# Optimization experiments

Hardware: AMD Instinct MI355X
Metric: run time of the kernel (lower is better)

## Reference

```python
import jax, jax.numpy as jnp
import numpy as np

B, N, NC = 16, 25200, 80          # batch, raw predictions, classes (COCO)
CONF_THRES = 0.25
IOU_THRES = 0.45
MAX_CAND = 1000                    # candidates kept after score top-k (pre-NMS)
CLS_OFFSET = 4096.0                # class-wise box offset (non-agnostic NMS trick)
EPS = 1e-7


def setup_inputs() -> dict:
    key = jax.random.key(0)
    # raw head output: [x, y, w, h, obj, cls0..cls79], values in [0,1]
    pred = jax.random.uniform(key, (B, N, 5 + NC), dtype=jnp.float32)
    return {"pred": pred}


def _xywh2xyxy(x):
    xy, wh = x[..., :2], x[..., 2:4]
    return jnp.concatenate([xy - wh * 0.5, xy + wh * 0.5], axis=-1)


def _box_iou(boxes):
    # boxes: [C, 4] xyxy -> pairwise IoU [C, C]
    area = (boxes[:, 2] - boxes[:, 0]) * (boxes[:, 3] - boxes[:, 1])
    lt = jnp.maximum(boxes[:, None, :2], boxes[None, :, :2])
    rb = jnp.minimum(boxes[:, None, 2:], boxes[None, :, 2:])
    wh = jnp.clip(rb - lt, 0.0)
    inter = wh[..., 0] * wh[..., 1]
    return inter / (area[:, None] + area[None, :] - inter + EPS)


def _nms_single(p):
    # p: [N, 5+NC] -> (out [MAX_CAND, 6] xyxy/conf/cls zero-padded, keep [MAX_CAND] bool)
    obj = p[:, 4]
    cls_scores = p[:, 5:] * obj[:, None]          # conf = obj * cls
    conf = jnp.max(cls_scores, axis=-1)
    cls_idx = jnp.argmax(cls_scores, axis=-1)
    valid = (obj > CONF_THRES) & (conf > CONF_THRES)
    score = jnp.where(valid, conf, -1.0)

    # pre-NMS top-k by score (sorted descending) — fixed-shape stand-in for boolean filter
    top_scores, idx = jax.lax.top_k(score, MAX_CAND)
    boxes = _xywh2xyxy(p[idx, :4])                # [C, 4]
    kconf = conf[idx]
    kcls = cls_idx[idx].astype(jnp.float32)
    valid_c = top_scores > 0.0

    # class-offset boxes so different classes never overlap (agnostic=False)
    off_boxes = boxes + kcls[:, None] * CLS_OFFSET
    iou = _box_iou(off_boxes)                     # [C, C]

    ar = jnp.arange(MAX_CAND)

    def body(i, keep):
        sup = keep[i] & (iou[i] > IOU_THRES) & (ar > i)
        return keep & jnp.logical_not(sup)

    keep = jax.lax.fori_loop(0, MAX_CAND, body, valid_c)

    out = jnp.concatenate([boxes, kconf[:, None], kcls[:, None]], axis=-1)  # [C, 6]
    out = jnp.where(keep[:, None], out, 0.0)
    return out, keep


def reference(pred):
    out, keep = jax.vmap(_nms_single)(pred)
    return out, keep
```

## Files before the change

kernel.cpp:

```cpp
#include <hip/hip_runtime.h>
#include <stdint.h>

typedef unsigned int u32;
typedef unsigned long long u64;

#define BATCH 16
#define NANCH 25200
#define NCLS 80
#define ROWF 85
#define MAXC 1000
#define CONF_T 0.25f
#define IOU_T 0.45f
#define EPS_F 1e-7f
#define TILE 64
#define NTILES ((NANCH + TILE - 1) / TILE)

__device__ __forceinline__ float iou_ref(float4 a, float4 b) {
#pragma clang fp contract(off)
  float ai = (a.z - a.x) * (a.w - a.y);
  float aj = (b.z - b.x) * (b.w - b.y);
  float ltx = fmaxf(a.x, b.x), lty = fmaxf(a.y, b.y);
  float rbx = fminf(a.z, b.z), rby = fminf(a.w, b.w);
  float wx = fmaxf(rbx - ltx, 0.0f), wy = fmaxf(rby - lty, 0.0f);
  float inter = wx * wy;
  return inter / (ai + aj - inter + EPS_F);
}

__global__ __launch_bounds__(256) void k1_score(const float* __restrict__ pred,
                                                u32* __restrict__ keys32) {
  __shared__ float srow[TILE * ROWF];
  __shared__ u32 skeys[TILE];
  int tid = threadIdx.x;
  int b = blockIdx.y;
  int t0 = blockIdx.x * TILE;
  int ntile = (t0 + TILE <= NANCH) ? TILE : (NANCH - t0);
  int nf4 = (ntile * ROWF) >> 2;

  const float4* src4 = (const float4*)(pred + ((size_t)b * NANCH + t0) * ROWF);
  float4* smem4 = (float4*)srow;
#pragma unroll
  for (int k = 0; k < 6; ++k) {
    int i = k * 256 + tid;
    if (i < nf4) smem4[i] = src4[i];
  }
  __syncthreads();

  int a = tid >> 2;
  int q = tid & 3;
  float best = -1e30f;
  int bidx = 0;
  float obj = 0.0f;
  if (a < ntile) {
    const float* row = srow + a * ROWF;
    obj = row[4];
    int c0 = q * 20;
#pragma unroll
    for (int c = 0; c < 20; ++c) {
      float s = row[5 + c0 + c] * obj;
      if (s > best) { best = s; bidx = c0 + c; }
    }
  }
#pragma unroll
  for (int off = 1; off < 4; off <<= 1) {
    float ob = __shfl_xor(best, off);
    int oi = __shfl_xor(bidx, off);
    if (ob > best || (ob == best && oi < bidx)) { best = ob; bidx = oi; }
  }
  if (q == 0 && a < ntile) {
    bool valid = (obj > CONF_T) && (best > CONF_T);
    u32 k = valid ? (((__float_as_uint(best) - 0x3E800000u) << 7) | (u32)bidx)
                  : 0u;
    skeys[a] = k;
  }
  __syncthreads();
  if (tid < ntile) keys32[(size_t)b * NANCH + t0 + tid] = skeys[tid];
}

__global__ __launch_bounds__(1024) void k2_select(const float* __restrict__ pred,
                                                  const u32* __restrict__ keys32,
                                                  float* __restrict__ selbox,
                                                  float* __restrict__ offbox,
                                                  float2* __restrict__ selmeta) {
  int b = blockIdx.x;
  int tid = threadIdx.x;
  int wv = tid >> 6, lane = tid & 63;
  __shared__ u32 h[8192];
  __shared__ u64 skey[2048];
  __shared__ u32 wsum[16];
  __shared__ u32 sh_fbin;
  __shared__ u32 scount;

  const u32* kb = keys32 + (size_t)b * NANCH;
  u32 kreg[25];
#pragma unroll
  for (int j = 0; j < 25; ++j) {
    int i = tid + j * 1024;
    kreg[j] = (i < NANCH) ? kb[i] : 0u;
  }
  for (int i = tid; i < 8192; i += 1024) h[i] = 0;
  if (tid == 0) { sh_fbin = 0; scount = 0; }
  skey[tid] = ~0ull;
  skey[tid + 1024] = ~0ull;
  __syncthreads();
#pragma unroll
  for (int j = 0; j < 25; ++j) {
    u32 k = kreg[j];
    if (k >= 0x80u) atomicAdd(&h[k >> 18], 1u);
  }
  __syncthreads();
  u32 a[8]; u32 lsum = 0;
#pragma unroll
  for (int k = 0; k < 8; ++k) { a[k] = h[8 * tid + k]; lsum += a[k]; }
  u32 suf = lsum;
#pragma unroll
  for (int off = 1; off < 64; off <<= 1) {
    u32 tv = __shfl_down(suf, off);
    if (lane + off < 64) suf += tv;
  }
  if (lane == 0) wsum[wv] = suf;
  __syncthreads();
  u32 base = 0;
#pragma unroll
  for (int w2 = 0; w2 < 16; ++w2) if (w2 > wv) base += wsum[w2];
  u32 e = base + suf - lsum;
#pragma unroll
  for (int k = 7; k >= 0; --k) {
    u32 inc = e + a[k];
    if ((int)inc >= MAXC && (int)e < MAXC) sh_fbin = (u32)(8 * tid + k);
    e = inc;
  }
  __syncthreads();
  u32 cut = sh_fbin << 18;
#pragma unroll
  for (int j = 0; j < 25; ++j) {
    u32 k = kreg[j];
    bool take = (k >= cut) && (k != 0u);
    u64 mask = __ballot(take ? 1 : 0);
    u32 wbase = 0;
    if (lane == 0 && mask != 0ull)
      wbase = atomicAdd(&scount, (u32)__popcll(mask));
    wbase = (u32)__shfl((int)wbase, 0);
    if (take) {
      int i = tid + j * 1024;
      u64 sk = ((u64)(k >> 7) << 32) |
               (u64)(((32767u - (u32)i) << 7) | (k & 127u));
      u32 p = wbase + (u32)__popcll(mask & ((1ull << lane) - 1ull));
      if (p < 2048) skey[p] = ~sk;
    }
  }
  __syncthreads();
  u64 v;
  if (scount <= 1024u) {
    v = skey[tid];
    for (u32 kk = 2; kk <= 1024; kk <<= 1) {
      for (u32 j = kk >> 1; j > 0; j >>= 1) {
        bool up = ((tid & kk) == 0);
        bool low = ((tid & j) == 0);
        if (j >= 64) {
          skey[tid] = v;
          __syncthreads();
          u64 o = skey[tid ^ j];
          bool takemin = (up == low);
          v = takemin ? (v < o ? v : o) : (v > o ? v : o);
          __syncthreads();
        } else {
          u64 o = __shfl_xor(v, (int)j);
          bool takemin = (up == low);
          v = takemin ? (v < o ? v : o) : (v > o ? v : o);
        }
      }
    }
  } else {
    for (u32 kk = 2; kk <= 2048; kk <<= 1) {
      for (u32 j = kk >> 1; j > 0; j >>= 1) {
        for (int idx = tid; idx < 2048; idx += 1024) {
          u32 ixj = (u32)idx ^ j;
          if (ixj > (u32)idx) {
            u64 x = skey[idx], y = skey[ixj];
            bool up = ((idx & kk) == 0);
            if (up ? (x > y) : (x < y)) { skey[idx] = y; skey[ixj] = x; }
          }
        }
        __syncthreads();
      }
    }
    v = skey[tid];
  }
  if (tid < MAXC) {
    u64 k = ~v;
    u32 confpart = (u32)(k >> 32);
    u32 lo = (u32)k;
    bool valid = confpart != 0u;
    float conf = 0.0f, x1 = 0.0f, y1 = 0.0f, x2 = 0.0f, y2 = 0.0f;
    float cf = 0.0f, offv = 0.0f;
    if (valid) {
      u32 nidx = 32767u - ((lo >> 7) & 0x7FFFu);
      u32 ci = lo & 127u;
      conf = __uint_as_float(confpart + 0x3E800000u);
      const float* pr = pred + ((size_t)b * NANCH + nidx) * ROWF;
      float x = pr[0], y = pr[1], w = pr[2], h2 = pr[3];
      x1 = x - w * 0.5f; y1 = y - h2 * 0.5f;
      x2 = x + w * 0.5f; y2 = y + h2 * 0.5f;
      cf = (float)ci; offv = cf * 4096.0f;
    }
    int o = b * MAXC + tid;
    ((float4*)selbox)[o] = make_float4(x1, y1, x2, y2);
    ((float4*)offbox)[o] = make_float4(x1 + offv, y1 + offv, x2 + offv, y2 + offv);
    selmeta[o] = make_float2(conf, cf);
  }
}

__global__ __launch_bounds__(256) void k3_dt(const float4* __restrict__ offbox4,
                                             u64* __restrict__ dt) {
  int wid = blockIdx.x * 4 + (threadIdx.x >> 6);
  int lane = threadIdx.x & 63;
  int b = wid / MAXC;
  int i = wid % MAXC;
  float4 bi = offbox4[b * MAXC + i];
  u64 myword = 0;
  int wmax = i >> 6;
  for (int w = 0; w <= wmax; ++w) {
    int j = w * 64 + lane;
    int jc = (j < MAXC) ? j : 0;
    float4 bj = offbox4[b * MAXC + jc];
    float iou = iou_ref(bi, bj);
    bool bit = (iou > IOU_T) && (j < i);
    u64 bal = __ballot(bit ? 1 : 0);
    if (lane == w) myword = bal;
  }
  if (lane < 16) dt[((size_t)b * 16 + lane) * MAXC + i] = myword;
}

__global__ __launch_bounds__(1024) void k4_jacobi(const u64* __restrict__ dt,
                                                  const float2* __restrict__ selmeta,
                                                  const float* __restrict__ selbox,
                                                  float* __restrict__ out) {
  int b = blockIdx.x;
  int tid = threadIdx.x;
  int wv = tid >> 6, lane = tid & 63;
  __shared__ u64 keepv[16];
  __shared__ u32 changed2[2];
  bool valid = false;
  float2 meta = make_float2(0.0f, 0.0f);
  u64 dtr[16];
  if (tid < MAXC) {
    meta = selmeta[b * MAXC + tid];
    valid = meta.x > 0.0f;
#pragma unroll
    for (int w = 0; w < 16; ++w) dtr[w] = dt[((size_t)b * 16 + w) * MAXC + tid];
  } else {
#pragma unroll
    for (int w = 0; w < 16; ++w) dtr[w] = 0ull;
  }
  u64 bal0 = __ballot(valid ? 1 : 0);
  if (tid == 0) { changed2[0] = 0; changed2[1] = 0; }
  if (lane == 0) keepv[wv] = bal0;
  __syncthreads();
  for (int pass = 0; pass < MAXC; ++pass) {
    u64 kv[16];
#pragma unroll
    for (int w = 0; w < 16; ++w) kv[w] = keepv[w];
    u64 s = 0;
#pragma unroll
    for (int w = 0; w < 16; ++w) s |= dtr[w] & kv[w];
    bool nk = valid && (s == 0ull);
    u64 bal = __ballot(nk ? 1 : 0);
    __syncthreads();
    if (lane == 0 && bal != kv[wv]) {
      keepv[wv] = bal;
      atomicOr(&changed2[pass & 1], 1u);
    }
    __syncthreads();
    u32 ch = changed2[pass & 1];
    if (tid == 0) changed2[(pass & 1) ^ 1] = 0;
    if (!ch) break;
  }
  if (tid < MAXC) {
    bool kept = ((keepv[wv] >> lane) & 1ull) != 0ull;
    size_t o = (size_t)b * MAXC + tid;
    float4 bx = ((const float4*)selbox)[o];
    float* orow = out + o * 6;
    orow[0] = kept ? bx.x : 0.0f;
    orow[1] = kept ? bx.y : 0.0f;
    orow[2] = kept ? bx.z : 0.0f;
    orow[3] = kept ? bx.w : 0.0f;
    orow[4] = kept ? meta.x : 0.0f;
    orow[5] = kept ? meta.y : 0.0f;
    out[(size_t)BATCH * MAXC * 6 + o] = kept ? 1.0f : 0.0f;
  }
}

extern "C" void kernel_launch(void* const* d_in, const int* in_sizes, int n_in,
                              void* d_out, int out_size, void* d_ws, size_t ws_size,
                              hipStream_t stream) {
  const float* pred = (const float*)d_in[0];
  float* out = (float*)d_out;
  char* ws = (char*)d_ws;
  size_t off = 0;
  auto alloc = [&](size_t bytes) -> void* {
    void* p = ws + off;
    off = (off + bytes + 255) & ~(size_t)255;
    return p;
  };
  u32* keys32   = (u32*)alloc((size_t)BATCH * NANCH * 4);
  float* selbox = (float*)alloc((size_t)BATCH * MAXC * 4 * 4);
  float* offbox = (float*)alloc((size_t)BATCH * MAXC * 4 * 4);
  float2* selmeta = (float2*)alloc((size_t)BATCH * MAXC * 8);
  u64* dt       = (u64*)alloc((size_t)BATCH * 16 * MAXC * 8);
  (void)ws_size; (void)in_sizes; (void)n_in; (void)out_size;

  dim3 g1(NTILES, BATCH);
  k1_score<<<g1, 256, 0, stream>>>(pred, keys32);
  k2_select<<<BATCH, 1024, 0, stream>>>(pred, keys32, selbox, offbox, selmeta);
  k3_dt<<<(BATCH * MAXC) / 4, 256, 0, stream>>>((const float4*)offbox, dt);
  k4_jacobi<<<BATCH, 1024, 0, stream>>>(dt, selmeta, selbox, out);
}
```

Measured before the change: 238.2 us.

## Fuse four NMS kernels into one cooperative persistent kernel with grid syncs

Replaces the four separate launches (score, select/sort, IoU bitmask, Jacobi keep iteration) with a single cooperative kernel of 256 blocks of 1024 threads, separated by grid.sync barriers. The aim is to remove per-launch overhead and inter-kernel gaps. In exchange, the score stage now runs with fewer, larger blocks, and the select and Jacobi stages still use only 16 blocks while the rest of the grid waits at the barrier. If the cooperative launch fails, it falls back to the old four-kernel path.

```diff
diff --git a/kernel.cpp b/kernel.cpp
--- a/kernel.cpp
+++ b/kernel.cpp
@@ -1,5 +1,8 @@
 #include <hip/hip_runtime.h>
+#include <hip/hip_cooperative_groups.h>
 #include <stdint.h>
+
+namespace cg = cooperative_groups;
 
 typedef unsigned int u32;
 typedef unsigned long long u64;
@@ -12,6 +15,13 @@
 #define CONF_T 0.25f
 #define IOU_T 0.45f
 #define EPS_F 1e-7f
+
+#define MBLK 1024
+#define MGRID 256
+#define TILE_A 256
+#define TPB ((NANCH + TILE_A - 1) / TILE_A)
+#define TT (TPB * BATCH)
+
 #define TILE 64
 #define NTILES ((NANCH + TILE - 1) / TILE)
 
@@ -26,6 +36,269 @@
   return inter / (ai + aj - inter + EPS_F);
 }
 
+struct SMa { float srow[TILE_A * ROWF]; u32 skeys[TILE_A]; };
+struct SMb { u32 h[8192]; u64 skey[2048]; u32 wsum[16]; u32 sh_fbin; u32 scount; };
+struct SMd { u64 keepv[16]; u32 changed2[2]; };
+union SMU { SMa a; SMb b; SMd d; };
+
+__global__ __launch_bounds__(MBLK) void mega(const float* __restrict__ pred,
+                                             u32* __restrict__ keys32,
+                                             float* __restrict__ selbox,
+                                             float* __restrict__ offbox,
+                                             float2* __restrict__ selmeta,
+                                             u64* __restrict__ dt,
+                                             float* __restrict__ out) {
+  cg::grid_group grid = cg::this_grid();
+  __shared__ SMU sm;
+  int tid = threadIdx.x;
+  int wv = tid >> 6, lane = tid & 63;
+
+  {
+    float4* smem4 = (float4*)sm.a.srow;
+    for (int t = blockIdx.x; t < TT; t += MGRID) {
+      int b = t / TPB;
+      int ti = t - b * TPB;
+      int t0 = ti * TILE_A;
+      int ntile = (t0 + TILE_A <= NANCH) ? TILE_A : (NANCH - t0);
+      int nf4 = (ntile * ROWF) >> 2;
+      const float4* src4 = (const float4*)(pred + ((size_t)b * NANCH + t0) * ROWF);
+      for (int i = tid; i < nf4; i += MBLK) smem4[i] = src4[i];
+      __syncthreads();
+      int a = tid >> 2;
+      int q = tid & 3;
+      float best = -1e30f;
+      int bidx = 0;
+      float obj = 0.0f;
+      if (a < ntile) {
+        const float* row = sm.a.srow + a * ROWF;
+        obj = row[4];
+        int c0 = q * 20;
+#pragma unroll
+        for (int c = 0; c < 20; ++c) {
+          float s = row[5 + c0 + c] * obj;
+          if (s > best) { best = s; bidx = c0 + c; }
+        }
+      }
+#pragma unroll
+      for (int off = 1; off < 4; off <<= 1) {
+        float ob = __shfl_xor(best, off);
+        int oi = __shfl_xor(bidx, off);
+        if (ob > best || (ob == best && oi < bidx)) { best = ob; bidx = oi; }
+      }
+      if (q == 0 && a < ntile) {
+        bool valid = (obj > CONF_T) && (best > CONF_T);
+        sm.a.skeys[a] = valid
+            ? (((__float_as_uint(best) - 0x3E800000u) << 7) | (u32)bidx) : 0u;
+      }
+      __syncthreads();
+      if (tid < ntile) keys32[(size_t)b * NANCH + t0 + tid] = sm.a.skeys[tid];
+      __syncthreads();
+    }
+  }
+  __threadfence();
+  grid.sync();
+
+  if (blockIdx.x < BATCH) {
+    int b = blockIdx.x;
+    const u32* kb = keys32 + (size_t)b * NANCH;
+    u32 kreg[25];
+#pragma unroll
+    for (int j = 0; j < 25; ++j) {
+      int i = tid + j * 1024;
+      kreg[j] = (i < NANCH) ? kb[i] : 0u;
+    }
+    for (int i = tid; i < 8192; i += 1024) sm.b.h[i] = 0;
+    if (tid == 0) { sm.b.sh_fbin = 0; sm.b.scount = 0; }
+    sm.b.skey[tid] = ~0ull;
+    sm.b.skey[tid + 1024] = ~0ull;
+    __syncthreads();
+#pragma unroll
+    for (int j = 0; j < 25; ++j) {
+      u32 k = kreg[j];
+      if (k >= 0x80u) atomicAdd(&sm.b.h[k >> 18], 1u);
+    }
+    __syncthreads();
+    u32 a[8]; u32 lsum = 0;
+#pragma unroll
+    for (int k = 0; k < 8; ++k) { a[k] = sm.b.h[8 * tid + k]; lsum += a[k]; }
+    u32 suf = lsum;
+#pragma unroll
+    for (int off = 1; off < 64; off <<= 1) {
+      u32 tv = __shfl_down(suf, off);
+      if (lane + off < 64) suf += tv;
+    }
+    if (lane == 0) sm.b.wsum[wv] = suf;
+    __syncthreads();
+    u32 base = 0;
+#pragma unroll
+    for (int w2 = 0; w2 < 16; ++w2) if (w2 > wv) base += sm.b.wsum[w2];
+    u32 e = base + suf - lsum;
+#pragma unroll
+    for (int k = 7; k >= 0; --k) {
+      u32 inc = e + a[k];
+      if ((int)inc >= MAXC && (int)e < MAXC) sm.b.sh_fbin = (u32)(8 * tid + k);
+      e = inc;
+    }
+    __syncthreads();
+    u32 cut = sm.b.sh_fbin << 18;
+#pragma unroll
+    for (int j = 0; j < 25; ++j) {
+      u32 k = kreg[j];
+      bool take = (k >= cut) && (k != 0u);
+      u64 mask = __ballot(take ? 1 : 0);
+      u32 wbase = 0;
+      if (lane == 0 && mask != 0ull)
+        wbase = atomicAdd(&sm.b.scount, (u32)__popcll(mask));
+      wbase = (u32)__shfl((int)wbase, 0);
+      if (take) {
+        int i = tid + j * 1024;
+        u64 sk = ((u64)(k >> 7) << 32) |
+                 (u64)(((32767u - (u32)i) << 7) | (k & 127u));
+        u32 p = wbase + (u32)__popcll(mask & ((1ull << lane) - 1ull));
+        if (p < 2048) sm.b.skey[p] = ~sk;
+      }
+    }
+    __syncthreads();
+    u64 v;
+    if (sm.b.scount <= 1024u) {
+      v = sm.b.skey[tid];
+      for (u32 kk = 2; kk <= 1024; kk <<= 1) {
+        for (u32 j = kk >> 1; j > 0; j >>= 1) {
+          bool up = ((tid & kk) == 0);
+          bool low = ((tid & j) == 0);
+          if (j >= 64) {
+            sm.b.skey[tid] = v;
+            __syncthreads();
+            u64 o = sm.b.skey[tid ^ j];
+            bool takemin = (up == low);
+            v = takemin ? (v < o ? v : o) : (v > o ? v : o);
+            __syncthreads();
+          } else {
+            u64 o = __shfl_xor(v, (int)j);
+            bool takemin = (up == low);
+            v = takemin ? (v < o ? v : o) : (v > o ? v : o);
+          }
+        }
+      }
+    } else {
+      for (u32 kk = 2; kk <= 2048; kk <<= 1) {
+        for (u32 j = kk >> 1; j > 0; j >>= 1) {
+          for (int idx = tid; idx < 2048; idx += 1024) {
+            u32 ixj = (u32)idx ^ j;
+            if (ixj > (u32)idx) {
+              u64 x = sm.b.skey[idx], y = sm.b.skey[ixj];
+              bool up = ((idx & kk) == 0);
+              if (up ? (x > y) : (x < y)) { sm.b.skey[idx] = y; sm.b.skey[ixj] = x; }
+            }
+          }
+          __syncthreads();
+        }
+      }
+      v = sm.b.skey[tid];
+    }
+    if (tid < MAXC) {
+      u64 k = ~v;
+      u32 confpart = (u32)(k >> 32);
+      u32 lo = (u32)k;
+      bool valid = confpart != 0u;
+      float conf = 0.0f, x1 = 0.0f, y1 = 0.0f, x2 = 0.0f, y2 = 0.0f;
+      float cf = 0.0f, offv = 0.0f;
+      if (valid) {
+        u32 nidx = 32767u - ((lo >> 7) & 0x7FFFu);
+        u32 ci = lo & 127u;
+        conf = __uint_as_float(confpart + 0x3E800000u);
+        const float* pr = pred + ((size_t)b * NANCH + nidx) * ROWF;
+        float x = pr[0], y = pr[1], w = pr[2], h2 = pr[3];
+        x1 = x - w * 0.5f; y1 = y - h2 * 0.5f;
+        x2 = x + w * 0.5f; y2 = y + h2 * 0.5f;
+        cf = (float)ci; offv = cf * 4096.0f;
+      }
+      int o = b * MAXC + tid;
+      ((float4*)selbox)[o] = make_float4(x1, y1, x2, y2);
+      ((float4*)offbox)[o] = make_float4(x1 + offv, y1 + offv, x2 + offv, y2 + offv);
+      selmeta[o] = make_float2(conf, cf);
+    }
+  }
+  __threadfence();
+  grid.sync();
+
+  {
+    const float4* offbox4 = (const float4*)offbox;
+    for (int wid = blockIdx.x * 16 + wv; wid < BATCH * MAXC; wid += MGRID * 16) {
+      int b = wid / MAXC;
+      int i = wid - b * MAXC;
+      float4 bi = offbox4[b * MAXC + i];
+      u64 myword = 0;
+      int wmax = i >> 6;
+      for (int w = 0; w <= wmax; ++w) {
+        int j = w * 64 + lane;
+        int jc = (j < MAXC) ? j : 0;
+        float4 bj = offbox4[b * MAXC + jc];
+        float iou = iou_ref(bi, bj);
+        bool bit = (iou > IOU_T) && (j < i);
+        u64 bal = __ballot(bit ? 1 : 0);
+        if (lane == w) myword = bal;
+      }
+      if (lane < 16) dt[((size_t)b * 16 + lane) * MAXC + i] = myword;
+    }
+  }
+  __threadfence();
+  grid.sync();
+
+  if (blockIdx.x < BATCH) {
+    int b = blockIdx.x;
+    bool valid = false;
+    float2 meta = make_float2(0.0f, 0.0f);
+    u64 dtr[16];
+    if (tid < MAXC) {
+      meta = selmeta[b * MAXC + tid];
+      valid = meta.x > 0.0f;
+#pragma unroll
+      for (int w = 0; w < 16; ++w) dtr[w] = dt[((size_t)b * 16 + w) * MAXC + tid];
+    } else {
+#pragma unroll
+      for (int w = 0; w < 16; ++w) dtr[w] = 0ull;
+    }
+    u64 bal0 = __ballot(valid ? 1 : 0);
+    if (tid == 0) { sm.d.changed2[0] = 0; sm.d.changed2[1] = 0; }
+    if (lane == 0) sm.d.keepv[wv] = bal0;
+    __syncthreads();
+    for (int pass = 0; pass < MAXC; ++pass) {
+      u64 kv[16];
+#pragma unroll
+      for (int w = 0; w < 16; ++w) kv[w] = sm.d.keepv[w];
+      u64 s = 0;
+#pragma unroll
+      for (int w = 0; w < 16; ++w) s |= dtr[w] & kv[w];
+      bool nk = valid && (s == 0ull);
+      u64 bal = __ballot(nk ? 1 : 0);
+      __syncthreads();
+      if (lane == 0 && bal != kv[wv]) {
+        sm.d.keepv[wv] = bal;
+        atomicOr(&sm.d.changed2[pass & 1], 1u);
+      }
+      __syncthreads();
+      u32 ch = sm.d.changed2[pass & 1];
+      if (tid == 0) sm.d.changed2[(pass & 1) ^ 1] = 0;
+      if (!ch) break;
+    }
+    if (tid < MAXC) {
+      bool kept = ((sm.d.keepv[wv] >> lane) & 1ull) != 0ull;
+      size_t o = (size_t)b * MAXC + tid;
+      float4 bx = ((const float4*)selbox)[o];
+      float* orow = out + o * 6;
+      orow[0] = kept ? bx.x : 0.0f;
+      orow[1] = kept ? bx.y : 0.0f;
+      orow[2] = kept ? bx.z : 0.0f;
+      orow[3] = kept ? bx.w : 0.0f;
+      orow[4] = kept ? meta.x : 0.0f;
+      orow[5] = kept ? meta.y : 0.0f;
+      out[(size_t)BATCH * MAXC * 6 + o] = kept ? 1.0f : 0.0f;
+    }
+  }
+}
+
+
 __global__ __launch_bounds__(256) void k1_score(const float* __restrict__ pred,
                                                 u32* __restrict__ keys32) {
   __shared__ float srow[TILE * ROWF];
@@ -35,7 +308,6 @@
   int t0 = blockIdx.x * TILE;
   int ntile = (t0 + TILE <= NANCH) ? TILE : (NANCH - t0);
   int nf4 = (ntile * ROWF) >> 2;
-
   const float4* src4 = (const float4*)(pred + ((size_t)b * NANCH + t0) * ROWF);
   float4* smem4 = (float4*)srow;
 #pragma unroll
@@ -44,9 +316,7 @@
     if (i < nf4) smem4[i] = src4[i];
   }
   __syncthreads();
-
-  int a = tid >> 2;
-  int q = tid & 3;
+  int a = tid >> 2, q = tid & 3;
   float best = -1e30f;
   int bidx = 0;
   float obj = 0.0f;
@@ -68,9 +338,7 @@
   }
   if (q == 0 && a < ntile) {
     bool valid = (obj > CONF_T) && (best > CONF_T);
-    u32 k = valid ? (((__float_as_uint(best) - 0x3E800000u) << 7) | (u32)bidx)
-                  : 0u;
-    skeys[a] = k;
+    skeys[a] = valid ? (((__float_as_uint(best) - 0x3E800000u) << 7) | (u32)bidx) : 0u;
   }
   __syncthreads();
   if (tid < ntile) keys32[(size_t)b * NANCH + t0 + tid] = skeys[tid];
@@ -89,7 +357,6 @@
   __shared__ u32 wsum[16];
   __shared__ u32 sh_fbin;
   __shared__ u32 scount;
-
   const u32* kb = keys32 + (size_t)b * NANCH;
   u32 kreg[25];
 #pragma unroll
@@ -309,9 +576,15 @@
   u64* dt       = (u64*)alloc((size_t)BATCH * 16 * MAXC * 8);
   (void)ws_size; (void)in_sizes; (void)n_in; (void)out_size;
 
-  dim3 g1(NTILES, BATCH);
-  k1_score<<<g1, 256, 0, stream>>>(pred, keys32);
-  k2_select<<<BATCH, 1024, 0, stream>>>(pred, keys32, selbox, offbox, selmeta);
-  k3_dt<<<(BATCH * MAXC) / 4, 256, 0, stream>>>((const float4*)offbox, dt);
-  k4_jacobi<<<BATCH, 1024, 0, stream>>>(dt, selmeta, selbox, out);
-}
+  void* args[] = { (void*)&pred, (void*)&keys32, (void*)&selbox, (void*)&offbox,
+                   (void*)&selmeta, (void*)&dt, (void*)&out };
+  hipError_t err = hipLaunchCooperativeKernel((const void*)mega, dim3(MGRID),
+                                              dim3(MBLK), args, 0, stream);
+  if (err != hipSuccess) {
+    dim3 g1(NTILES, BATCH);
+    k1_score<<<g1, 256, 0, stream>>>(pred, keys32);
+    k2_select<<<BATCH, 1024, 0, stream>>>(pred, keys32, selbox, offbox, selmeta);
+    k3_dt<<<(BATCH * MAXC) / 4, 256, 0, stream>>>((const float4*)offbox, dt);
+    k4_jacobi<<<BATCH, 1024, 0, stream>>>(dt, selmeta, selbox, out);
+  }
+}
```

New measurement: 564.8 us. 137% more time.

## Fuse select, IoU bitmask, and Jacobi NMS kernels into one per-batch kernel

Applied to the files above, without the earlier changes.

Merges the top-k selection, IoU suppression-matrix construction, and iterative keep-mask kernels into a single 1024-thread block per batch image. Boxes and the suppression bitmask now stay in shared memory (union-overlaid with the selection scratch), and box/meta values stay in registers instead of going through global workspace buffers. This removes two kernel launches and the global round trips, but the IoU matrix is now built by only 16 waves per batch on 16 blocks rather than spread across 4000 blocks. The large shared footprint (~147KB) also limits occupancy.

```diff
diff --git a/kernel.cpp b/kernel.cpp
--- a/kernel.cpp
+++ b/kernel.cpp
@@ -76,19 +76,19 @@
   if (tid < ntile) keys32[(size_t)b * NANCH + t0 + tid] = skeys[tid];
 }
 
-__global__ __launch_bounds__(1024) void k2_select(const float* __restrict__ pred,
-                                                  const u32* __restrict__ keys32,
-                                                  float* __restrict__ selbox,
-                                                  float* __restrict__ offbox,
-                                                  float2* __restrict__ selmeta) {
+struct SMsel { u32 h[8192]; u64 skey[2048]; u32 wsum[16]; u32 sh_fbin; u32 scount; };
+struct SMnms { float4 boxes[1024]; u64 dtm[16][1025]; };
+union SMU2 { SMsel sel; SMnms nms; };
+
+__global__ __launch_bounds__(1024) void k234(const float* __restrict__ pred,
+                                             const u32* __restrict__ keys32,
+                                             float* __restrict__ out) {
   int b = blockIdx.x;
   int tid = threadIdx.x;
   int wv = tid >> 6, lane = tid & 63;
-  __shared__ u32 h[8192];
-  __shared__ u64 skey[2048];
-  __shared__ u32 wsum[16];
-  __shared__ u32 sh_fbin;
-  __shared__ u32 scount;
+  __shared__ SMU2 sm;
+  __shared__ u64 keepv[16];
+  __shared__ u32 changed2[2];
 
   const u32* kb = keys32 + (size_t)b * NANCH;
   u32 kreg[25];
@@ -97,40 +97,40 @@
     int i = tid + j * 1024;
     kreg[j] = (i < NANCH) ? kb[i] : 0u;
   }
-  for (int i = tid; i < 8192; i += 1024) h[i] = 0;
-  if (tid == 0) { sh_fbin = 0; scount = 0; }
-  skey[tid] = ~0ull;
-  skey[tid + 1024] = ~0ull;
+  for (int i = tid; i < 8192; i += 1024) sm.sel.h[i] = 0;
+  if (tid == 0) { sm.sel.sh_fbin = 0; sm.sel.scount = 0; }
+  sm.sel.skey[tid] = ~0ull;
+  sm.sel.skey[tid + 1024] = ~0ull;
   __syncthreads();
 #pragma unroll
   for (int j = 0; j < 25; ++j) {
     u32 k = kreg[j];
-    if (k >= 0x80u) atomicAdd(&h[k >> 18], 1u);
+    if (k >= 0x80u) atomicAdd(&sm.sel.h[k >> 18], 1u);
   }
   __syncthreads();
   u32 a[8]; u32 lsum = 0;
 #pragma unroll
-  for (int k = 0; k < 8; ++k) { a[k] = h[8 * tid + k]; lsum += a[k]; }
+  for (int k = 0; k < 8; ++k) { a[k] = sm.sel.h[8 * tid + k]; lsum += a[k]; }
   u32 suf = lsum;
 #pragma unroll
   for (int off = 1; off < 64; off <<= 1) {
     u32 tv = __shfl_down(suf, off);
     if (lane + off < 64) suf += tv;
   }
-  if (lane == 0) wsum[wv] = suf;
+  if (lane == 0) sm.sel.wsum[wv] = suf;
   __syncthreads();
   u32 base = 0;
 #pragma unroll
-  for (int w2 = 0; w2 < 16; ++w2) if (w2 > wv) base += wsum[w2];
+  for (int w2 = 0; w2 < 16; ++w2) if (w2 > wv) base += sm.sel.wsum[w2];
   u32 e = base + suf - lsum;
 #pragma unroll
   for (int k = 7; k >= 0; --k) {
     u32 inc = e + a[k];
-    if ((int)inc >= MAXC && (int)e < MAXC) sh_fbin = (u32)(8 * tid + k);
+    if ((int)inc >= MAXC && (int)e < MAXC) sm.sel.sh_fbin = (u32)(8 * tid + k);
     e = inc;
   }
   __syncthreads();
-  u32 cut = sh_fbin << 18;
+  u32 cut = sm.sel.sh_fbin << 18;
 #pragma unroll
   for (int j = 0; j < 25; ++j) {
     u32 k = kreg[j];
@@ -138,28 +138,28 @@
     u64 mask = __ballot(take ? 1 : 0);
     u32 wbase = 0;
     if (lane == 0 && mask != 0ull)
-      wbase = atomicAdd(&scount, (u32)__popcll(mask));
+      wbase = atomicAdd(&sm.sel.scount, (u32)__popcll(mask));
     wbase = (u32)__shfl((int)wbase, 0);
     if (take) {
       int i = tid + j * 1024;
       u64 sk = ((u64)(k >> 7) << 32) |
                (u64)(((32767u - (u32)i) << 7) | (k & 127u));
       u32 p = wbase + (u32)__popcll(mask & ((1ull << lane) - 1ull));
-      if (p < 2048) skey[p] = ~sk;
+      if (p < 2048) sm.sel.skey[p] = ~sk;
     }
   }
   __syncthreads();
   u64 v;
-  if (scount <= 1024u) {
-    v = skey[tid];
+  if (sm.sel.scount <= 1024u) {
+    v = sm.sel.skey[tid];
     for (u32 kk = 2; kk <= 1024; kk <<= 1) {
       for (u32 j = kk >> 1; j > 0; j >>= 1) {
         bool up = ((tid & kk) == 0);
         bool low = ((tid & j) == 0);
         if (j >= 64) {
-          skey[tid] = v;
+          sm.sel.skey[tid] = v;
           __syncthreads();
-          u64 o = skey[tid ^ j];
+          u64 o = sm.sel.skey[tid ^ j];
           bool takemin = (up == low);
           v = takemin ? (v < o ? v : o) : (v > o ? v : o);
           __syncthreads();
@@ -176,83 +176,66 @@
         for (int idx = tid; idx < 2048; idx += 1024) {
           u32 ixj = (u32)idx ^ j;
           if (ixj > (u32)idx) {
-            u64 x = skey[idx], y = skey[ixj];
+            u64 x = sm.sel.skey[idx], y = sm.sel.skey[ixj];
             bool up = ((idx & kk) == 0);
-            if (up ? (x > y) : (x < y)) { skey[idx] = y; skey[ixj] = x; }
+            if (up ? (x > y) : (x < y)) { sm.sel.skey[idx] = y; sm.sel.skey[ixj] = x; }
           }
         }
         __syncthreads();
       }
     }
-    v = skey[tid];
+    v = sm.sel.skey[tid];
+  }
+  __syncthreads();
+
+  u64 kk2 = ~v;
+  u32 confpart = (u32)(kk2 >> 32);
+  u32 lo = (u32)kk2;
+  bool valid = (tid < MAXC) && (confpart != 0u);
+  float conf = 0.0f, x1 = 0.0f, y1 = 0.0f, x2 = 0.0f, y2 = 0.0f, cf = 0.0f;
+  if (valid) {
+    u32 nidx = 32767u - ((lo >> 7) & 0x7FFFu);
+    u32 ci = lo & 127u;
+    conf = __uint_as_float(confpart + 0x3E800000u);
+    const float* pr = pred + ((size_t)b * NANCH + nidx) * ROWF;
+    float x = pr[0], y = pr[1], w = pr[2], h2 = pr[3];
+    x1 = x - w * 0.5f; y1 = y - h2 * 0.5f;
+    x2 = x + w * 0.5f; y2 = y + h2 * 0.5f;
+    cf = (float)ci;
   }
   if (tid < MAXC) {
-    u64 k = ~v;
-    u32 confpart = (u32)(k >> 32);
-    u32 lo = (u32)k;
-    bool valid = confpart != 0u;
-    float conf = 0.0f, x1 = 0.0f, y1 = 0.0f, x2 = 0.0f, y2 = 0.0f;
-    float cf = 0.0f, offv = 0.0f;
-    if (valid) {
-      u32 nidx = 32767u - ((lo >> 7) & 0x7FFFu);
-      u32 ci = lo & 127u;
-      conf = __uint_as_float(confpart + 0x3E800000u);
-      const float* pr = pred + ((size_t)b * NANCH + nidx) * ROWF;
-      float x = pr[0], y = pr[1], w = pr[2], h2 = pr[3];
-      x1 = x - w * 0.5f; y1 = y - h2 * 0.5f;
-      x2 = x + w * 0.5f; y2 = y + h2 * 0.5f;
-      cf = (float)ci; offv = cf * 4096.0f;
-    }
-    int o = b * MAXC + tid;
-    ((float4*)selbox)[o] = make_float4(x1, y1, x2, y2);
-    ((float4*)offbox)[o] = make_float4(x1 + offv, y1 + offv, x2 + offv, y2 + offv);
-    selmeta[o] = make_float2(conf, cf);
-  }
-}
-
-__global__ __launch_bounds__(256) void k3_dt(const float4* __restrict__ offbox4,
-                                             u64* __restrict__ dt) {
-  int wid = blockIdx.x * 4 + (threadIdx.x >> 6);
-  int lane = threadIdx.x & 63;
-  int b = wid / MAXC;
-  int i = wid % MAXC;
-  float4 bi = offbox4[b * MAXC + i];
-  u64 myword = 0;
-  int wmax = i >> 6;
-  for (int w = 0; w <= wmax; ++w) {
-    int j = w * 64 + lane;
-    int jc = (j < MAXC) ? j : 0;
-    float4 bj = offbox4[b * MAXC + jc];
-    float iou = iou_ref(bi, bj);
-    bool bit = (iou > IOU_T) && (j < i);
-    u64 bal = __ballot(bit ? 1 : 0);
-    if (lane == w) myword = bal;
-  }
-  if (lane < 16) dt[((size_t)b * 16 + lane) * MAXC + i] = myword;
-}
-
-__global__ __launch_bounds__(1024) void k4_jacobi(const u64* __restrict__ dt,
-                                                  const float2* __restrict__ selmeta,
-                                                  const float* __restrict__ selbox,
-                                                  float* __restrict__ out) {
-  int b = blockIdx.x;
-  int tid = threadIdx.x;
-  int wv = tid >> 6, lane = tid & 63;
-  __shared__ u64 keepv[16];
-  __shared__ u32 changed2[2];
-  bool valid = false;
-  float2 meta = make_float2(0.0f, 0.0f);
+    float offv = cf * 4096.0f;
+    sm.nms.boxes[tid] = make_float4(x1 + offv, y1 + offv, x2 + offv, y2 + offv);
+  }
+  __syncthreads();
+
+  for (int i = wv; i < MAXC; i += 16) {
+    float4 bi = sm.nms.boxes[i];
+    u64 myword = 0;
+    int wmax = i >> 6;
+    for (int w = 0; w <= wmax; ++w) {
+      int j = w * 64 + lane;
+      int jc = (j < MAXC) ? j : 0;
+      float4 bj = sm.nms.boxes[jc];
+      float iou = iou_ref(bi, bj);
+      bool bit = (iou > IOU_T) && (j < i);
+      u64 bal = __ballot(bit ? 1 : 0);
+      if (lane == w) myword = bal;
+    }
+    if (lane < 16) sm.nms.dtm[lane][i] = myword;
+  }
+  __syncthreads();
+
   u64 dtr[16];
   if (tid < MAXC) {
-    meta = selmeta[b * MAXC + tid];
-    valid = meta.x > 0.0f;
-#pragma unroll
-    for (int w = 0; w < 16; ++w) dtr[w] = dt[((size_t)b * 16 + w) * MAXC + tid];
+#pragma unroll
+    for (int w = 0; w < 16; ++w) dtr[w] = sm.nms.dtm[w][tid];
   } else {
 #pragma unroll
     for (int w = 0; w < 16; ++w) dtr[w] = 0ull;
   }
-  u64 bal0 = __ballot(valid ? 1 : 0);
+  bool validk = valid && (conf > 0.0f);
+  u64 bal0 = __ballot(validk ? 1 : 0);
   if (tid == 0) { changed2[0] = 0; changed2[1] = 0; }
   if (lane == 0) keepv[wv] = bal0;
   __syncthreads();
@@ -263,7 +246,7 @@
     u64 s = 0;
 #pragma unroll
     for (int w = 0; w < 16; ++w) s |= dtr[w] & kv[w];
-    bool nk = valid && (s == 0ull);
+    bool nk = validk && (s == 0ull);
     u64 bal = __ballot(nk ? 1 : 0);
     __syncthreads();
     if (lane == 0 && bal != kv[wv]) {
@@ -278,14 +261,13 @@
   if (tid < MAXC) {
     bool kept = ((keepv[wv] >> lane) & 1ull) != 0ull;
     size_t o = (size_t)b * MAXC + tid;
-    float4 bx = ((const float4*)selbox)[o];
     float* orow = out + o * 6;
-    orow[0] = kept ? bx.x : 0.0f;
-    orow[1] = kept ? bx.y : 0.0f;
-    orow[2] = kept ? bx.z : 0.0f;
-    orow[3] = kept ? bx.w : 0.0f;
-    orow[4] = kept ? meta.x : 0.0f;
-    orow[5] = kept ? meta.y : 0.0f;
+    orow[0] = kept ? x1 : 0.0f;
+    orow[1] = kept ? y1 : 0.0f;
+    orow[2] = kept ? x2 : 0.0f;
+    orow[3] = kept ? y2 : 0.0f;
+    orow[4] = kept ? conf : 0.0f;
+    orow[5] = kept ? cf : 0.0f;
     out[(size_t)BATCH * MAXC * 6 + o] = kept ? 1.0f : 0.0f;
   }
 }
@@ -296,22 +278,10 @@
   const float* pred = (const float*)d_in[0];
   float* out = (float*)d_out;
   char* ws = (char*)d_ws;
-  size_t off = 0;
-  auto alloc = [&](size_t bytes) -> void* {
-    void* p = ws + off;
-    off = (off + bytes + 255) & ~(size_t)255;
-    return p;
-  };
-  u32* keys32   = (u32*)alloc((size_t)BATCH * NANCH * 4);
-  float* selbox = (float*)alloc((size_t)BATCH * MAXC * 4 * 4);
-  float* offbox = (float*)alloc((size_t)BATCH * MAXC * 4 * 4);
-  float2* selmeta = (float2*)alloc((size_t)BATCH * MAXC * 8);
-  u64* dt       = (u64*)alloc((size_t)BATCH * 16 * MAXC * 8);
+  u32* keys32 = (u32*)ws;
   (void)ws_size; (void)in_sizes; (void)n_in; (void)out_size;
 
   dim3 g1(NTILES, BATCH);
   k1_score<<<g1, 256, 0, stream>>>(pred, keys32);
-  k2_select<<<BATCH, 1024, 0, stream>>>(pred, keys32, selbox, offbox, selmeta);
-  k3_dt<<<(BATCH * MAXC) / 4, 256, 0, stream>>>((const float4*)offbox, dt);
-  k4_jacobi<<<BATCH, 1024, 0, stream>>>(dt, selmeta, selbox, out);
-}
+  k234<<<BATCH, 1024, 0, stream>>>(pred, keys32, out);
+}
```

After: 361.5 us. 51.8% more time.
